# Kernel tuning notes

Hardware: AMD Instinct MI355X
Metric: run time of the kernel (lower is better)

Reference implementation:

```python
import jax, jax.numpy as jnp
import numpy as np
from jax import lax

EPS = 1e-06


def _ema_scan(x, s):
    # x: [B, C, T]; s: [C] smoothing coeff in [0, 1]
    # Recurrence: y_0 = x_0; y_t = s * x_t + (1 - s) * y_{t-1}
    # Expressed as affine pairs (A_t, b_t) with y_t = A_t * y_{t-1} + b_t
    s_b = s[None, :, None]  # [1, C, 1]
    A0 = jnp.zeros_like(x[:, :, :1])
    A_rest = jnp.broadcast_to(1.0 - s_b, x[:, :, 1:].shape)
    A = jnp.concatenate([A0, A_rest], axis=2)
    b = jnp.concatenate([x[:, :, :1], s_b * x[:, :, 1:]], axis=2)

    def combine(c1, c2):
        a1, b1 = c1
        a2, b2 = c2
        return (a1 * a2, a2 * b1 + b2)

    _, ema = lax.associative_scan(combine, (A, b), axis=2)
    return ema


def setup_inputs() -> dict:
    key = jax.random.key(0)
    B, C, T = 32, 128, 16000
    kx, = jax.random.split(key, 1)
    x = jax.random.uniform(kx, (B, C, T), dtype=jnp.float32)
    alpha = jnp.ones((C,), dtype=jnp.float32) * 0.96
    delta = jnp.ones((C,), dtype=jnp.float32) * 2.0
    root = jnp.ones((C,), dtype=jnp.float32) * 2.0
    ema_weights = jnp.ones((C,), dtype=jnp.float32) * 0.04
    return {"x": x, "alpha": alpha, "delta": delta, "root": root, "ema_weights": ema_weights}


def reference(x, alpha, delta, root, ema_weights):
    # sPCEN: per-channel EMA smoother + power-law compression
    s = jnp.clip(ema_weights, 0.0, 1.0)
    ema = _ema_scan(x, s)  # [B, C, T]

    alpha_c = jnp.minimum(alpha, 1.0)[None, :, None]
    root_c = jnp.maximum(root, 1.0)[None, :, None]
    r = 1.0 / root_c
    d = delta[None, :, None]

    out = (x / (EPS + ema) ** alpha_c + d) ** r - d ** r
    return out
```

## Files before the change

kernel.cpp:

```cpp
#include <hip/hip_runtime.h>
#include <math.h>

#define T_LEN   16000
#define THREADS 256
#define CHUNK   63
#define EPS_F   1e-6f

__launch_bounds__(THREADS)
__global__ void pcen_kernel(const float* __restrict__ x,
                            const float* __restrict__ alpha,
                            const float* __restrict__ delta,
                            const float* __restrict__ root,
                            const float* __restrict__ ema_w,
                            float* __restrict__ out, int C) {
    __shared__ __align__(16) float buf[T_LEN];
    __shared__ float swA[4], swB[4];

    const int row = blockIdx.x;
    const int c   = row % C;
    const int tid = threadIdx.x;

    const float s   = fminf(fmaxf(ema_w[c], 0.0f), 1.0f);
    const float q   = 1.0f - s;
    const float a_c = fminf(alpha[c], 1.0f);
    const float r   = 1.0f / fmaxf(root[c], 1.0f);
    const float d   = delta[c];
    const float dr  = powf(d, r);

    const float* xr   = x   + (size_t)row * T_LEN;
    float*       outr = out + (size_t)row * T_LEN;

    const float4* x4 = (const float4*)xr;
    float4*       b4 = (float4*)buf;
    for (int i = tid; i < T_LEN / 4; i += THREADS) b4[i] = x4[i];
    __syncthreads();

    const int base = tid * CHUNK;
    const int end  = min(base + CHUNK, T_LEN);
    float a = 1.0f, b = 0.0f;
    for (int g = base; g < end; ++g) {
        float xv = buf[g];
        float xa = (g == 0) ? 0.0f : q;
        float xb = (g == 0) ? xv   : s * xv;
        b = fmaf(xa, b, xb);
        a *= xa;
    }

    const int lane = tid & 63;
    const int wave = tid >> 6;
    float la = a, lb = b;
    #pragma unroll
    for (int off = 1; off < 64; off <<= 1) {
        float ua = __shfl_up(la, off);
        float ub = __shfl_up(lb, off);
        if (lane >= off) {
            lb = fmaf(la, ub, lb);
            la *= ua;
        }
    }

    if (lane == 63) { swA[wave] = la; swB[wave] = lb; }
    __syncthreads();
    float pb = 0.0f;
    #pragma unroll
    for (int w = 0; w < 3; ++w) {
        if (w < wave) pb = fmaf(swA[w], pb, swB[w]);
    }

    float ea = __shfl_up(la, 1);
    float eb = __shfl_up(lb, 1);
    float e_in = (lane == 0) ? pb : fmaf(ea, pb, eb);

    float e = e_in;
    for (int g = base; g < end; ++g) {
        float xv = buf[g];
        e = (g == 0) ? xv : fmaf(q, e, s * xv);
        float t  = exp2f(a_c * log2f(EPS_F + e));
        float o  = exp2f(r * log2f(xv / t + d)) - dr;
        buf[g] = o;
    }
    __syncthreads();

    float4* o4 = (float4*)outr;
    for (int i = tid; i < T_LEN / 4; i += THREADS) o4[i] = b4[i];
}

extern "C" void kernel_launch(void* const* d_in, const int* in_sizes, int n_in,
                              void* d_out, int out_size, void* d_ws, size_t ws_size,
                              hipStream_t stream) {
    const float* x     = (const float*)d_in[0];
    const float* alpha = (const float*)d_in[1];
    const float* delta = (const float*)d_in[2];
    const float* root  = (const float*)d_in[3];
    const float* ema_w = (const float*)d_in[4];
    float* out = (float*)d_out;

    const int C    = in_sizes[1];
    const int rows = in_sizes[0] / T_LEN;

    pcen_kernel<<<rows, THREADS, 0, stream>>>(x, alpha, delta, root, ema_w, out, C);
}
```

Baseline: 549.7 us.

## Tile time axis into four LDS chunks with carried EMA state

Instead of staging the whole 16000-sample row in 64KB of LDS, the row is processed in four tiles of 4352 samples (17 per thread), with the EMA state carried between tiles via a block-level affine scan. This shrinks LDS per block so more blocks can be resident per CU (launch bounds request 4), improving latency hiding for the memory-bound row loads. It also fully unrolls the per-thread chunk loops and replaces the division x/t with a log-domain subtraction. The cost is extra barriers and scan work per tile, plus padding of the last tile with ones.

```diff
diff --git a/kernel.cpp b/kernel.cpp
--- a/kernel.cpp
+++ b/kernel.cpp
@@ -1,24 +1,30 @@
 #include <hip/hip_runtime.h>
 #include <math.h>
 
-#define T_LEN   16000
-#define THREADS 256
-#define CHUNK   63
-#define EPS_F   1e-6f
+#define T_LEN    16000
+#define T_LEN4   4000
+#define THREADS  256
+#define CHUNK    17
+#define TILE     (THREADS * CHUNK)
+#define TILE4    (TILE / 4)
+#define NT       4
+#define EPS_F    1e-6f
 
-__launch_bounds__(THREADS)
+__launch_bounds__(THREADS, 4)
 __global__ void pcen_kernel(const float* __restrict__ x,
                             const float* __restrict__ alpha,
                             const float* __restrict__ delta,
                             const float* __restrict__ root,
                             const float* __restrict__ ema_w,
                             float* __restrict__ out, int C) {
-    __shared__ __align__(16) float buf[T_LEN];
+    __shared__ __align__(16) float buf[TILE];
     __shared__ float swA[4], swB[4];
 
-    const int row = blockIdx.x;
-    const int c   = row % C;
-    const int tid = threadIdx.x;
+    const int row  = blockIdx.x;
+    const int c    = row % C;
+    const int tid  = threadIdx.x;
+    const int lane = tid & 63;
+    const int wave = tid >> 6;
 
     const float s   = fminf(fmaxf(ema_w[c], 0.0f), 1.0f);
     const float q   = 1.0f - s;
@@ -27,62 +33,87 @@
     const float d   = delta[c];
     const float dr  = powf(d, r);
 
-    const float* xr   = x   + (size_t)row * T_LEN;
-    float*       outr = out + (size_t)row * T_LEN;
+    const float4* x4 = (const float4*)(x   + (size_t)row * T_LEN);
+    float4*       o4 = (float4*)      (out + (size_t)row * T_LEN);
+    float4*       b4 = (float4*)buf;
 
-    const float4* x4 = (const float4*)xr;
-    float4*       b4 = (float4*)buf;
-    for (int i = tid; i < T_LEN / 4; i += THREADS) b4[i] = x4[i];
-    __syncthreads();
+    float e_carry = 0.0f;
+    const int lbase = tid * CHUNK;
 
-    const int base = tid * CHUNK;
-    const int end  = min(base + CHUNK, T_LEN);
-    float a = 1.0f, b = 0.0f;
-    for (int g = base; g < end; ++g) {
-        float xv = buf[g];
-        float xa = (g == 0) ? 0.0f : q;
-        float xb = (g == 0) ? xv   : s * xv;
-        b = fmaf(xa, b, xb);
-        a *= xa;
+    for (int t = 0; t < NT; ++t) {
+        const int tb4 = t * TILE4;
+
+        #pragma unroll
+        for (int k = 0; k < 5; ++k) {
+            int i4l = tid + k * THREADS;
+            if (i4l < TILE4) {
+                int i4 = tb4 + i4l;
+                b4[i4l] = (i4 < T_LEN4) ? x4[i4] : make_float4(1.f, 1.f, 1.f, 1.f);
+            }
+        }
+        __syncthreads();
+
+        float a = 1.0f, b = 0.0f;
+        #pragma unroll
+        for (int j = 0; j < CHUNK; ++j) {
+            float xv = buf[lbase + j];
+            bool first = (t == 0) & (tid == 0) & (j == 0);
+            float xa = first ? 0.0f : q;
+            float xb = first ? xv   : s * xv;
+            b = fmaf(xa, b, xb);
+            a *= xa;
+        }
+
+        float la = a, lb = b;
+        #pragma unroll
+        for (int off = 1; off < 64; off <<= 1) {
+            float ua = __shfl_up(la, off);
+            float ub = __shfl_up(lb, off);
+            if (lane >= off) { lb = fmaf(la, ub, lb); la *= ua; }
+        }
+        if (lane == 63) { swA[wave] = la; swB[wave] = lb; }
+        __syncthreads();
+
+        float pa = 1.0f, pb = 0.0f;
+        #pragma unroll
+        for (int w = 0; w < 3; ++w) {
+            if (w < wave) { pb = fmaf(swA[w], pb, swB[w]); pa *= swA[w]; }
+        }
+        float ea = __shfl_up(la, 1);
+        float eb = __shfl_up(lb, 1);
+        float a_ex, b_ex;
+        if (lane == 0) { a_ex = pa;      b_ex = pb; }
+        else           { a_ex = pa * ea; b_ex = fmaf(ea, pb, eb); }
+        float e = fmaf(a_ex, e_carry, b_ex);
+
+        float ta = 1.0f, tb = 0.0f;
+        #pragma unroll
+        for (int w = 0; w < 4; ++w) { tb = fmaf(swA[w], tb, swB[w]); ta *= swA[w]; }
+        e_carry = fmaf(ta, e_carry, tb);
+
+        #pragma unroll
+        for (int j = 0; j < CHUNK; ++j) {
+            float xv = buf[lbase + j];
+            bool first = (t == 0) & (tid == 0) & (j == 0);
+            e = first ? xv : fmaf(q, e, s * xv);
+            float lge = log2f(EPS_F + e);
+            float lgx = log2f(xv);
+            float v   = exp2f(fmaf(-a_c, lge, lgx));
+            float o   = exp2f(r * log2f(v + d)) - dr;
+            buf[lbase + j] = o;
+        }
+        __syncthreads();
+
+        #pragma unroll
+        for (int k = 0; k < 5; ++k) {
+            int i4l = tid + k * THREADS;
+            if (i4l < TILE4) {
+                int i4 = tb4 + i4l;
+                if (i4 < T_LEN4) o4[i4] = b4[i4l];
+            }
+        }
+        __syncthreads();
     }
-
-    const int lane = tid & 63;
-    const int wave = tid >> 6;
-    float la = a, lb = b;
-    #pragma unroll
-    for (int off = 1; off < 64; off <<= 1) {
-        float ua = __shfl_up(la, off);
-        float ub = __shfl_up(lb, off);
-        if (lane >= off) {
-            lb = fmaf(la, ub, lb);
-            la *= ua;
-        }
-    }
-
-    if (lane == 63) { swA[wave] = la; swB[wave] = lb; }
-    __syncthreads();
-    float pb = 0.0f;
-    #pragma unroll
-    for (int w = 0; w < 3; ++w) {
-        if (w < wave) pb = fmaf(swA[w], pb, swB[w]);
-    }
-
-    float ea = __shfl_up(la, 1);
-    float eb = __shfl_up(lb, 1);
-    float e_in = (lane == 0) ? pb : fmaf(ea, pb, eb);
-
-    float e = e_in;
-    for (int g = base; g < end; ++g) {
-        float xv = buf[g];
-        e = (g == 0) ? xv : fmaf(q, e, s * xv);
-        float t  = exp2f(a_c * log2f(EPS_F + e));
-        float o  = exp2f(r * log2f(xv / t + d)) - dr;
-        buf[g] = o;
-    }
-    __syncthreads();
-
-    float4* o4 = (float4*)outr;
-    for (int i = tid; i < T_LEN / 4; i += THREADS) o4[i] = b4[i];
 }
 
 extern "C" void kernel_launch(void* const* d_in, const int* in_sizes, int n_in,
```

Result: faster. 453.0 us (-17.6%).
